# Kernel optimization log

Measured on AMD Instinct MI355X. Metric: run time of the kernel, lower is better.

The kernel has to match this reference:

```python
import jax, jax.numpy as jnp
import numpy as np

# Static module configuration (matches init_kwargs)
B, CIN, COUT, K, H, W = 4, 32, 32, 3, 128, 128
UM = 2                      # um_dim: 2D vector fields
NW = ((K - 1) // 2) * 4     # num_weights = radius*4 = 4


def setup_inputs() -> dict:
    key = jax.random.key(0)
    k1, k2, k3 = jax.random.split(key, 3)
    params = jax.random.normal(k1, (COUT, CIN, NW, 4), jnp.float32)
    basis = jax.random.normal(k2, (NW, 4, K, K, UM, UM), jnp.float32)
    # Replicate the init-time scaling of the torch module:
    # std over the (non-zero) outer-product kernel, then scale params and basis.
    init_kernel = jnp.einsum('abcd,cdefgh->abcdefgh', params, basis)
    stds = jnp.std(init_kernel)  # random basis -> all entries nonzero
    scaler = jnp.sqrt(0.6 / (np.sqrt(CIN) * (K ** 2) * stds))
    params = params * scaler
    basis = basis * scaler
    bias_term = jnp.ones((1, COUT, 2, 1, 1), jnp.float32) / 100.0
    b = jnp.float32(0.01)
    xx = jax.random.normal(k3, (B, CIN * UM, H, W), jnp.float32)
    return {'xx': xx, 'params': params, 'basis': basis,
            'bias_term': bias_term, 'b': b}


def _forward(xx, params, basis, bias_term, b):
    Bn, C, Hh, Ww = xx.shape
    I, O = CIN, COUT
    # --- get_kernel: einsum + transposes -> conv weight (O*2, I*2, K, K) ---
    Kr = jnp.einsum('abcd,cdefgh->abefgh', params, basis)      # (O,I,K,K,2,2)
    kernel = jnp.transpose(Kr, (0, 4, 1, 5, 2, 3)).reshape(O * 2, I * 2, K, K)
    # --- unfold with replicate padding: P[b,c,kh,kw,h,w] ---
    xp = jnp.pad(xx, ((0, 0), (0, 0), (1, 1), (1, 1)), mode='edge')
    P = jnp.stack([xp[:, :, i:i + Hh, j:j + Ww]
                   for i in range(K) for j in range(K)], axis=2)
    P = P.reshape(Bn, C, K, K, Hh, Ww)
    # --- per-window mean subtraction over (input_channels, kh, kw) ---
    P5 = P.reshape(Bn, I, UM, K, K, Hh, Ww)
    avgs = P5.mean(axis=(1, 3, 4), keepdims=True)              # (B,1,2,1,1,H,W)
    P = (P5 - avgs).reshape(Bn, C, K, K, Hh, Ww)
    avgs = avgs[:, :, :, 0, 0]                                 # (B,1,2,H,W)
    # --- strided conv2d on the blown-up grid == this einsum:
    # big[b,c,3h+di,3w+dj] = P[b,c,kh=dj,kw=di,h,w], so kernel (di,dj)=(p,q)
    # pairs with patch (kh=q, kw=p).
    out = jnp.einsum('bcqphw,ocpq->bohw', P, kernel)           # (B,O*2,H,W)
    out = out.reshape(Bn, O, 2, Hh, Ww) + bias_term
    # --- 'relu' vector activation: normalize, zero where norm <= b ---
    norm = jnp.sqrt(out[:, :, 0] ** 2 + out[:, :, 1] ** 2)[:, :, None]
    out = jnp.where(norm - b <= 0.0, 0.0, out / norm)
    # --- add_mean ---
    out = out + avgs
    return out.reshape(Bn, O * 2, Hh, Ww)


def reference(xx, params, basis, bias_term, b):
    return _forward(xx, params, basis, bias_term, b)
```

## Files before the change

kernel.cpp:

```cpp
#include <hip/hip_runtime.h>

#define BN 4
#define CH 64
#define HH 128
#define WW 128
#define PIX (HH*WW)

#define OFF_WL  0
#define OFF_S   36864
#define OFF_CS  36992
#define OFF_AVG 168064

__global__ void k_weights(const float* __restrict__ params,
                          const float* __restrict__ basis,
                          float* __restrict__ Wl) {
    int idx = blockIdx.x * blockDim.x + threadIdx.x;
    if (idx >= 64 * 9 * 64) return;
    int oc  = idx & 63;
    int tap = (idx >> 6) % 9;
    int c   = idx / (64 * 9);
    int q = tap / 3, p = tap % 3;
    int o = oc >> 1, g = oc & 1;
    int i = c >> 1, u = c & 1;
    float s = 0.f;
    #pragma unroll
    for (int n = 0; n < 4; ++n)
        #pragma unroll
        for (int d = 0; d < 4; ++d)
            s = fmaf(params[((o * 32 + i) * 4 + n) * 4 + d],
                     basis[((((n * 4 + d) * 3 + p) * 3 + q) * 2 + g) * 2 + u], s);
    Wl[idx] = s;
}

__global__ void k_ssum(const float* __restrict__ Wl, float* __restrict__ S) {
    int t = threadIdx.x;
    if (t >= 128) return;
    int u = t >> 6, oc = t & 63;
    float s = 0.f;
    for (int i = 0; i < 32; ++i)
        for (int tap = 0; tap < 9; ++tap)
            s += Wl[((i * 2 + u) * 9 + tap) * 64 + oc];
    S[t] = s;
}

__global__ void k_colsum(const float* __restrict__ x, float* __restrict__ cs) {
    int idx = blockIdx.x * blockDim.x + threadIdx.x;
    if (idx >= BN * 2 * PIX) return;
    int pix = idx & (PIX - 1);
    int u   = (idx >> 14) & 1;
    int b   = idx >> 15;
    const float* xb = x + b * CH * PIX + u * PIX + pix;
    float s = 0.f;
    #pragma unroll
    for (int i = 0; i < 32; ++i) s += xb[i * 2 * PIX];
    cs[idx] = s;
}

__global__ void k_avg(const float* __restrict__ cs, float* __restrict__ avg) {
    int idx = blockIdx.x * blockDim.x + threadIdx.x;
    if (idx >= BN * 2 * PIX) return;
    int w  = idx & (WW - 1);
    int h  = (idx >> 7) & (HH - 1);
    int bu = idx >> 14;
    const float* c0 = cs + bu * PIX;
    int hm = h > 0 ? h - 1 : 0, hp = h < HH - 1 ? h + 1 : HH - 1;
    int wm = w > 0 ? w - 1 : 0, wp = w < WW - 1 ? w + 1 : WW - 1;
    float s = c0[hm * WW + wm] + c0[hm * WW + w] + c0[hm * WW + wp]
            + c0[h  * WW + wm] + c0[h  * WW + w] + c0[h  * WW + wp]
            + c0[hp * WW + wm] + c0[hp * WW + w] + c0[hp * WW + wp];
    avg[idx] = s * (1.0f / 288.0f);
}

__global__ __launch_bounds__(256) void k_main(
    const float* __restrict__ x,
    const float* __restrict__ Wl,
    const float* __restrict__ S,
    const float* __restrict__ bias,
    const float* __restrict__ avg,
    const float* __restrict__ bptr,
    float* __restrict__ out)
{
    int tile   = blockIdx.x;
    int ocbase = blockIdx.y * 16;
    int b      = blockIdx.z;
    int ty = threadIdx.x >> 4, tx = threadIdx.x & 15;
    int h = (tile >> 3) * 16 + ty;
    int w = (tile & 7) * 16 + tx;

    int hm = h > 0 ? h - 1 : 0, hp = h < HH - 1 ? h + 1 : HH - 1;
    int wm = w > 0 ? w - 1 : 0, wp = w < WW - 1 ? w + 1 : WW - 1;
    int rowoff[3] = { hm * WW, h * WW, hp * WW };
    int coloff[3] = { wm, w, wp };

    float acc[16];
    #pragma unroll
    for (int j = 0; j < 16; ++j) acc[j] = 0.f;

    const float* xc = x + b * CH * PIX;
    const float* wc = Wl + ocbase;
    for (int c = 0; c < CH; ++c) {
        float xv[9];
        #pragma unroll
        for (int q = 0; q < 3; ++q)
            #pragma unroll
            for (int p = 0; p < 3; ++p)
                xv[q * 3 + p] = xc[rowoff[q] + coloff[p]];
        #pragma unroll
        for (int t = 0; t < 9; ++t) {
            #pragma unroll
            for (int j = 0; j < 16; ++j)
                acc[j] = fmaf(xv[t], wc[t * 64 + j], acc[j]);
        }
        xc += PIX;
        wc += 9 * 64;
    }

    int pix = h * WW + w;
    float a0 = avg[(b * 2 + 0) * PIX + pix];
    float a1 = avg[(b * 2 + 1) * PIX + pix];
    float bthr = bptr[0];

    float t[16];
    #pragma unroll
    for (int j = 0; j < 16; ++j) {
        int oc = ocbase + j;
        t[j] = acc[j] - a0 * S[oc] - a1 * S[64 + oc] + bias[oc];
    }

    float* ob = out + b * CH * PIX + pix;
    #pragma unroll
    for (int j = 0; j < 16; j += 2) {
        float n = sqrtf(t[j] * t[j] + t[j + 1] * t[j + 1]);
        float r0, r1;
        if (n - bthr <= 0.f) { r0 = 0.f; r1 = 0.f; }
        else { r0 = t[j] / n; r1 = t[j + 1] / n; }
        ob[(ocbase + j)     * PIX] = r0 + a0;
        ob[(ocbase + j + 1) * PIX] = r1 + a1;
    }
}

extern "C" void kernel_launch(void* const* d_in, const int* in_sizes, int n_in,
                              void* d_out, int out_size, void* d_ws, size_t ws_size,
                              hipStream_t stream) {
    const float* xx     = (const float*)d_in[0];
    const float* params = (const float*)d_in[1];
    const float* basis  = (const float*)d_in[2];
    const float* bias   = (const float*)d_in[3];
    const float* bptr   = (const float*)d_in[4];
    float* out = (float*)d_out;
    float* ws  = (float*)d_ws;

    float* Wl  = ws + OFF_WL;
    float* S   = ws + OFF_S;
    float* cs  = ws + OFF_CS;
    float* avg = ws + OFF_AVG;

    k_weights<<<(64 * 9 * 64 + 255) / 256, 256, 0, stream>>>(params, basis, Wl);
    k_ssum<<<1, 128, 0, stream>>>(Wl, S);
    k_colsum<<<(BN * 2 * PIX + 255) / 256, 256, 0, stream>>>(xx, cs);
    k_avg<<<(BN * 2 * PIX + 255) / 256, 256, 0, stream>>>(cs, avg);

    dim3 grid(64, 4, BN);
    k_main<<<grid, 256, 0, stream>>>(xx, Wl, S, bias, avg, bptr, out);
}
```

Before: 146.3 us.

## Register-block two rows per thread, prefetch next channel, merge prep kernels

```diff
diff --git a/kernel.cpp b/kernel.cpp
--- a/kernel.cpp
+++ b/kernel.cpp
@@ -11,64 +11,77 @@
 #define OFF_CS  36992
 #define OFF_AVG 168064
 
-__global__ void k_weights(const float* __restrict__ params,
-                          const float* __restrict__ basis,
-                          float* __restrict__ Wl) {
-    int idx = blockIdx.x * blockDim.x + threadIdx.x;
-    if (idx >= 64 * 9 * 64) return;
-    int oc  = idx & 63;
-    int tap = (idx >> 6) % 9;
-    int c   = idx / (64 * 9);
-    int q = tap / 3, p = tap % 3;
-    int o = oc >> 1, g = oc & 1;
-    int i = c >> 1, u = c & 1;
-    float s = 0.f;
-    #pragma unroll
-    for (int n = 0; n < 4; ++n)
-        #pragma unroll
-        for (int d = 0; d < 4; ++d)
-            s = fmaf(params[((o * 32 + i) * 4 + n) * 4 + d],
-                     basis[((((n * 4 + d) * 3 + p) * 3 + q) * 2 + g) * 2 + u], s);
-    Wl[idx] = s;
-}
-
-__global__ void k_ssum(const float* __restrict__ Wl, float* __restrict__ S) {
-    int t = threadIdx.x;
-    if (t >= 128) return;
-    int u = t >> 6, oc = t & 63;
-    float s = 0.f;
-    for (int i = 0; i < 32; ++i)
-        for (int tap = 0; tap < 9; ++tap)
+__global__ __launch_bounds__(256) void k_prep1(const float* __restrict__ params,
+                                               const float* __restrict__ basis,
+                                               const float* __restrict__ x,
+                                               float* __restrict__ Wl,
+                                               float* __restrict__ cs) {
+    int bx = blockIdx.x;
+    if (bx < 144) {
+        int idx = bx * 256 + threadIdx.x;
+        int oc  = idx & 63;
+        int tap = (idx >> 6) % 9;
+        int c   = idx / 576;
+        int q = tap / 3, p = tap % 3;
+        int o = oc >> 1, g = oc & 1;
+        int i = c >> 1, u = c & 1;
+        float s = 0.f;
+        #pragma unroll
+        for (int n = 0; n < 4; ++n)
+            #pragma unroll
+            for (int d = 0; d < 4; ++d)
+                s = fmaf(params[((o * 32 + i) * 4 + n) * 4 + d],
+                         basis[((((n * 4 + d) * 3 + p) * 3 + q) * 2 + g) * 2 + u], s);
+        Wl[idx] = s;
+    } else {
+        int idx = (bx - 144) * 256 + threadIdx.x;
+        int pq  = idx & (PIX / 4 - 1);
+        int u   = (idx >> 12) & 1;
+        int b   = idx >> 13;
+        const float4* xb = (const float4*)x;
+        float4 s = make_float4(0.f, 0.f, 0.f, 0.f);
+        #pragma unroll
+        for (int i = 0; i < 32; ++i) {
+            float4 v = xb[(size_t)(b * CH + 2 * i + u) * (PIX / 4) + pq];
+            s.x += v.x; s.y += v.y; s.z += v.z; s.w += v.w;
+        }
+        ((float4*)cs)[(b * 2 + u) * (PIX / 4) + pq] = s;
+    }
+}
+
+__global__ __launch_bounds__(256) void k_prep2(const float* __restrict__ Wl,
+                                               const float* __restrict__ cs,
+                                               float* __restrict__ S,
+                                               float* __restrict__ avg) {
+    __shared__ float red[4];
+    int bx = blockIdx.x;
+    if (bx < 128) {
+        int u = bx >> 6, oc = bx & 63;
+        int t = threadIdx.x;
+        float s = 0.f;
+        for (int k = t; k < 288; k += 256) {
+            int i = k / 9, tap = k - i * 9;
             s += Wl[((i * 2 + u) * 9 + tap) * 64 + oc];
-    S[t] = s;
-}
-
-__global__ void k_colsum(const float* __restrict__ x, float* __restrict__ cs) {
-    int idx = blockIdx.x * blockDim.x + threadIdx.x;
-    if (idx >= BN * 2 * PIX) return;
-    int pix = idx & (PIX - 1);
-    int u   = (idx >> 14) & 1;
-    int b   = idx >> 15;
-    const float* xb = x + b * CH * PIX + u * PIX + pix;
-    float s = 0.f;
-    #pragma unroll
-    for (int i = 0; i < 32; ++i) s += xb[i * 2 * PIX];
-    cs[idx] = s;
-}
-
-__global__ void k_avg(const float* __restrict__ cs, float* __restrict__ avg) {
-    int idx = blockIdx.x * blockDim.x + threadIdx.x;
-    if (idx >= BN * 2 * PIX) return;
-    int w  = idx & (WW - 1);
-    int h  = (idx >> 7) & (HH - 1);
-    int bu = idx >> 14;
-    const float* c0 = cs + bu * PIX;
-    int hm = h > 0 ? h - 1 : 0, hp = h < HH - 1 ? h + 1 : HH - 1;
-    int wm = w > 0 ? w - 1 : 0, wp = w < WW - 1 ? w + 1 : WW - 1;
-    float s = c0[hm * WW + wm] + c0[hm * WW + w] + c0[hm * WW + wp]
-            + c0[h  * WW + wm] + c0[h  * WW + w] + c0[h  * WW + wp]
-            + c0[hp * WW + wm] + c0[hp * WW + w] + c0[hp * WW + wp];
-    avg[idx] = s * (1.0f / 288.0f);
+        }
+        #pragma unroll
+        for (int o = 32; o; o >>= 1) s += __shfl_down(s, o, 64);
+        int lane = t & 63, wv = t >> 6;
+        if (lane == 0) red[wv] = s;
+        __syncthreads();
+        if (t == 0) S[bx] = red[0] + red[1] + red[2] + red[3];
+    } else {
+        int idx = (bx - 128) * 256 + threadIdx.x;
+        int w  = idx & (WW - 1);
+        int h  = (idx >> 7) & (HH - 1);
+        int bu = idx >> 14;
+        const float* c0 = cs + bu * PIX;
+        int hm = h > 0 ? h - 1 : 0, hp = h < HH - 1 ? h + 1 : HH - 1;
+        int wm = w > 0 ? w - 1 : 0, wp = w < WW - 1 ? w + 1 : WW - 1;
+        float s = c0[hm * WW + wm] + c0[hm * WW + w] + c0[hm * WW + wp]
+                + c0[h  * WW + wm] + c0[h  * WW + w] + c0[h  * WW + wp]
+                + c0[hp * WW + wm] + c0[hp * WW + w] + c0[hp * WW + wp];
+        avg[idx] = s * (1.0f / 288.0f);
+    }
 }
 
 __global__ __launch_bounds__(256) void k_main(
@@ -83,59 +96,92 @@
     int tile   = blockIdx.x;
     int ocbase = blockIdx.y * 16;
     int b      = blockIdx.z;
-    int ty = threadIdx.x >> 4, tx = threadIdx.x & 15;
-    int h = (tile >> 3) * 16 + ty;
-    int w = (tile & 7) * 16 + tx;
-
-    int hm = h > 0 ? h - 1 : 0, hp = h < HH - 1 ? h + 1 : HH - 1;
+    int tx = threadIdx.x & 15, ty = threadIdx.x >> 4;
+    int w  = (tile & 7) * 16 + tx;
+    int h0 = (tile >> 3) * 32 + ty * 2;
+
+    int rm = h0 > 0 ? h0 - 1 : 0;
+    int r3 = (h0 + 2 < HH) ? h0 + 2 : HH - 1;
+    int rowoff[4] = { rm * WW, h0 * WW, (h0 + 1) * WW, r3 * WW };
     int wm = w > 0 ? w - 1 : 0, wp = w < WW - 1 ? w + 1 : WW - 1;
-    int rowoff[3] = { hm * WW, h * WW, hp * WW };
     int coloff[3] = { wm, w, wp };
 
-    float acc[16];
-    #pragma unroll
-    for (int j = 0; j < 16; ++j) acc[j] = 0.f;
-
-    const float* xc = x + b * CH * PIX;
+    int off[12];
+    #pragma unroll
+    for (int r = 0; r < 4; ++r)
+        #pragma unroll
+        for (int p = 0; p < 3; ++p)
+            off[r * 3 + p] = rowoff[r] + coloff[p];
+
+    float acc0[16], acc1[16];
+    #pragma unroll
+    for (int j = 0; j < 16; ++j) { acc0[j] = 0.f; acc1[j] = 0.f; }
+
+    const float* xc = x + (size_t)b * CH * PIX;
     const float* wc = Wl + ocbase;
+
+    float xv[12];
+    #pragma unroll
+    for (int k = 0; k < 12; ++k) xv[k] = xc[off[k]];
+
     for (int c = 0; c < CH; ++c) {
-        float xv[9];
-        #pragma unroll
-        for (int q = 0; q < 3; ++q)
+        const float* xn = xc + (c < CH - 1 ? PIX : 0);
+        float xf[12];
+        #pragma unroll
+        for (int k = 0; k < 12; ++k) xf[k] = xn[off[k]];
+
+        #pragma unroll
+        for (int q = 0; q < 3; ++q) {
             #pragma unroll
-            for (int p = 0; p < 3; ++p)
-                xv[q * 3 + p] = xc[rowoff[q] + coloff[p]];
-        #pragma unroll
-        for (int t = 0; t < 9; ++t) {
-            #pragma unroll
-            for (int j = 0; j < 16; ++j)
-                acc[j] = fmaf(xv[t], wc[t * 64 + j], acc[j]);
+            for (int p = 0; p < 3; ++p) {
+                float x0 = xv[q * 3 + p];
+                float x1 = xv[(q + 1) * 3 + p];
+                const float* wt = wc + (q * 3 + p) * 64;
+                #pragma unroll
+                for (int j = 0; j < 16; ++j) {
+                    float wv = wt[j];
+                    acc0[j] = fmaf(x0, wv, acc0[j]);
+                    acc1[j] = fmaf(x1, wv, acc1[j]);
+                }
+            }
         }
+        #pragma unroll
+        for (int k = 0; k < 12; ++k) xv[k] = xf[k];
         xc += PIX;
-        wc += 9 * 64;
-    }
-
-    int pix = h * WW + w;
-    float a0 = avg[(b * 2 + 0) * PIX + pix];
-    float a1 = avg[(b * 2 + 1) * PIX + pix];
+        wc += 576;
+    }
+
+    int pix0 = h0 * WW + w;
+    float a0p0 = avg[(b * 2 + 0) * PIX + pix0];
+    float a1p0 = avg[(b * 2 + 1) * PIX + pix0];
+    float a0p1 = avg[(b * 2 + 0) * PIX + pix0 + WW];
+    float a1p1 = avg[(b * 2 + 1) * PIX + pix0 + WW];
     float bthr = bptr[0];
 
-    float t[16];
-    #pragma unroll
-    for (int j = 0; j < 16; ++j) {
+    float* ob = out + (size_t)b * CH * PIX + pix0;
+    #pragma unroll
+    for (int j = 0; j < 16; j += 2) {
         int oc = ocbase + j;
-        t[j] = acc[j] - a0 * S[oc] - a1 * S[64 + oc] + bias[oc];
-    }
-
-    float* ob = out + b * CH * PIX + pix;
-    #pragma unroll
-    for (int j = 0; j < 16; j += 2) {
-        float n = sqrtf(t[j] * t[j] + t[j + 1] * t[j + 1]);
+        float s0 = S[oc], s1 = S[oc + 1];
+        float su0 = S[64 + oc], su1 = S[64 + oc + 1];
+        float bi0 = bias[oc], bi1 = bias[oc + 1];
+
+        float t0 = acc0[j]     - a0p0 * s0 - a1p0 * su0 + bi0;
+        float t1 = acc0[j + 1] - a0p0 * s1 - a1p0 * su1 + bi1;
+        float n = sqrtf(t0 * t0 + t1 * t1);
         float r0, r1;
         if (n - bthr <= 0.f) { r0 = 0.f; r1 = 0.f; }
-        else { r0 = t[j] / n; r1 = t[j + 1] / n; }
-        ob[(ocbase + j)     * PIX] = r0 + a0;
-        ob[(ocbase + j + 1) * PIX] = r1 + a1;
+        else { r0 = t0 / n; r1 = t1 / n; }
+        ob[(size_t)oc * PIX]       = r0 + a0p0;
+        ob[(size_t)(oc + 1) * PIX] = r1 + a1p0;
+
+        t0 = acc1[j]     - a0p1 * s0 - a1p1 * su0 + bi0;
+        t1 = acc1[j + 1] - a0p1 * s1 - a1p1 * su1 + bi1;
+        n = sqrtf(t0 * t0 + t1 * t1);
+        if (n - bthr <= 0.f) { r0 = 0.f; r1 = 0.f; }
+        else { r0 = t0 / n; r1 = t1 / n; }
+        ob[(size_t)oc * PIX + WW]       = r0 + a0p1;
+        ob[(size_t)(oc + 1) * PIX + WW] = r1 + a1p1;
     }
 }
 
@@ -155,11 +201,9 @@
     float* cs  = ws + OFF_CS;
     float* avg = ws + OFF_AVG;
 
-    k_weights<<<(64 * 9 * 64 + 255) / 256, 256, 0, stream>>>(params, basis, Wl);
-    k_ssum<<<1, 128, 0, stream>>>(Wl, S);
-    k_colsum<<<(BN * 2 * PIX + 255) / 256, 256, 0, stream>>>(xx, cs);
-    k_avg<<<(BN * 2 * PIX + 255) / 256, 256, 0, stream>>>(cs, avg);
-
-    dim3 grid(64, 4, BN);
+    k_prep1<<<272, 256, 0, stream>>>(params, basis, xx, Wl, cs);
+    k_prep2<<<640, 256, 0, stream>>>(Wl, cs, S, avg);
+
+    dim3 grid(32, 4, BN);
     k_main<<<grid, 256, 0, stream>>>(xx, Wl, S, bias, avg, bptr, out);
 }
```

Measured after the change: 150.5 us. 2.9% more time.
